# Kernel tuning notes

Hardware: AMD Instinct MI355X
Metric: run time of the kernel (lower is better)

The kernel has to match this reference:

```python
import jax, jax.numpy as jnp
import numpy as np

S, B, H, V = 512, 512, 256, 128


def setup_inputs() -> dict:
    key = jax.random.key(0)
    ks = jax.random.split(key, 11)
    sd = 0.05
    return {
        "x": jax.random.randint(ks[0], (S, B), 0, V, dtype=jnp.int32),
        "w_ih0": jax.random.normal(ks[1], (4 * H, 1), jnp.float32) * sd,
        "w_hh0": jax.random.normal(ks[2], (4 * H, H), jnp.float32) * sd,
        "b_ih0": jax.random.normal(ks[3], (4 * H,), jnp.float32) * sd,
        "b_hh0": jax.random.normal(ks[4], (4 * H,), jnp.float32) * sd,
        "w_ih1": jax.random.normal(ks[5], (4 * H, H), jnp.float32) * sd,
        "w_hh1": jax.random.normal(ks[6], (4 * H, H), jnp.float32) * sd,
        "b_ih1": jax.random.normal(ks[7], (4 * H,), jnp.float32) * sd,
        "b_hh1": jax.random.normal(ks[8], (4 * H,), jnp.float32) * sd,
        "W_out": jax.random.normal(ks[9], (V, H), jnp.float32) * sd,
        "b_out": jax.random.normal(ks[10], (V,), jnp.float32) * sd,
    }


def _lstm_cell(x_t, h, c, w_ih, w_hh, b_ih, b_hh):
    # PyTorch gate order: i, f, g, o
    gates = x_t @ w_ih.T + h @ w_hh.T + b_ih + b_hh  # [B, 4H]
    i, f, g, o = jnp.split(gates, 4, axis=-1)
    c_new = jax.nn.sigmoid(f) * c + jax.nn.sigmoid(i) * jnp.tanh(g)
    h_new = jax.nn.sigmoid(o) * jnp.tanh(c_new)
    return h_new, c_new


def reference(x, w_ih0, w_hh0, b_ih0, b_hh0, w_ih1, w_hh1, b_ih1, b_hh1, W_out, b_out):
    s, b = x.shape
    xf = x.astype(jnp.float32)[..., None]  # [S, B, 1] raw token ids as floats

    def step(carry, x_t):
        h0, c0, h1, c1 = carry
        h0, c0 = _lstm_cell(x_t, h0, c0, w_ih0, w_hh0, b_ih0, b_hh0)
        h1, c1 = _lstm_cell(h0, h1, c1, w_ih1, w_hh1, b_ih1, b_hh1)
        return (h0, c0, h1, c1), h1

    z = jnp.zeros((b, w_hh0.shape[1]), jnp.float32)
    _, hs = jax.lax.scan(step, (z, z, z, z), xf)  # hs: [S, B, H]
    return hs @ W_out.T + b_out  # [S, B, V]
```

## Files before the change

### kernel.cpp

```cpp
#include <hip/hip_runtime.h>


#define S_ 512
#define B_ 512
#define H_ 256
#define V_ 128

typedef _Float16 f16;
typedef __attribute__((ext_vector_type(8))) _Float16 f16x8;
typedef __attribute__((ext_vector_type(4))) float f32x4;
typedef unsigned long long u64;
typedef unsigned u32;
typedef unsigned short u16;

#define OFF_B0   0
#define OFF_B1   524288
#define OFF_BP   1572864
#define OFF_EX   1638400

__device__ __forceinline__ float sigm(float z) { return 1.0f / (1.0f + __expf(-z)); }
__device__ __forceinline__ float tanh_fast(float z) {
  return 2.0f / (1.0f + __expf(-2.0f * z)) - 1.0f;
}

__global__ void prep_kernel(const float* __restrict__ w_hh0,
                            const float* __restrict__ w_ih1, const float* __restrict__ w_hh1,
                            const float* __restrict__ W_out, void* __restrict__ ws) {
  int idx = blockIdx.x * blockDim.x + threadIdx.x;
  f16* wsh = (f16*)ws;
  if (idx < 32768) {
    int j = idx >> 12, w = (idx >> 9) & 7, kk = (idx >> 6) & 7, lane = idx & 63;
    int gate = w >> 1, half = w & 1;
    int hcol = j * 32 + half * 16 + (lane & 15);
    int G = gate * H_ + hcol;
    int k0 = kk * 32 + (lane >> 4) * 8;
    f16x8 v;
    #pragma unroll
    for (int i = 0; i < 8; ++i) v[i] = (f16)w_hh0[G * H_ + k0 + i];
    *(f16x8*)(wsh + idx * 8) = v;
  } else if (idx < 32768 + 65536) {
    int t = idx - 32768;
    int j = t >> 13, w = (t >> 10) & 7, kk = (t >> 6) & 15, lane = t & 63;
    int gate = w >> 1, half = w & 1;
    int hcol = j * 32 + half * 16 + (lane & 15);
    int G = gate * H_ + hcol;
    int k0 = kk * 32 + (lane >> 4) * 8;
    const float* src = (k0 < H_) ? (w_ih1 + G * H_ + k0) : (w_hh1 + G * H_ + (k0 - H_));
    f16x8 v;
    #pragma unroll
    for (int i = 0; i < 8; ++i) v[i] = (f16)src[i];
    *(f16x8*)(wsh + 262144 + t * 8) = v;
  } else if (idx < 32768 + 65536 + 4096) {
    int t = idx - (32768 + 65536);
    int j = t >> 9, w = (t >> 6) & 7, lane = t & 63;
    int vcol = j * 16 + (lane & 15);
    int k0 = w * 32 + (lane >> 4) * 8;
    f16x8 v;
    #pragma unroll
    for (int i = 0; i < 8; ++i) v[i] = (f16)W_out[vcol * H_ + k0 + i];
    *(f16x8*)(wsh + 786432 + t * 8) = v;
  } else if (idx < 102400 + 262144) {
    ((u64*)((char*)ws + OFF_EX))[idx - 102400] = 0ull;
  }
}

__device__ __forceinline__ u64 aload64(const u64* p) {
  return __hip_atomic_load((u64*)p, __ATOMIC_RELAXED, __HIP_MEMORY_SCOPE_AGENT);
}
__device__ __forceinline__ void astore32(u32* p, u32 v) {
  __hip_atomic_store(p, v, __ATOMIC_RELAXED, __HIP_MEMORY_SCOPE_AGENT);
}

__device__ __forceinline__ u32 pack2(u64 q) {
  return (u32)(q & 0xffffu) | (((u32)(q >> 32)) << 16);
}

__device__ __forceinline__ f16x8 afrag(const f16* buf, int lane, int kk) {
  return *(const f16x8*)(buf + kk * 512 + lane * 8);
}

__global__ __launch_bounds__(512, 2) void lstm_r11(const int* __restrict__ x,
                                                   const f16* __restrict__ wts,
                                                   u32* __restrict__ ex,
                                                   const float* __restrict__ w_ih0,
                                                   const float* __restrict__ b_ih0,
                                                   const float* __restrict__ b_hh0,
                                                   const float* __restrict__ b_ih1,
                                                   const float* __restrict__ b_hh1,
                                                   const float* __restrict__ b_out,
                                                   float* __restrict__ out) {
  __shared__ __align__(16) f16 H0[4096], H1[4096];
  __shared__ __align__(16) float gsc0[4][16][33];
  __shared__ __align__(16) float gsc1[4][16][33];
  __shared__ __align__(16) float ppart[4][8][64];

  const int tid  = threadIdx.x;
  const int lane = tid & 63;
  const int w    = tid >> 6;
  const int bg   = blockIdx.x >> 3;
  const int j    = blockIdx.x & 7;

  f16x8 B0r[8], B1r[16], BPr;
  {
    const f16* p0 = wts + (size_t)(j * 8 + w) * 8 * 512 + lane * 8;
    #pragma unroll
    for (int kk = 0; kk < 8; ++kk) B0r[kk] = *(const f16x8*)(p0 + kk * 512);
    const f16* p1 = wts + 262144 + (size_t)(j * 8 + w) * 16 * 512 + lane * 8;
    #pragma unroll
    for (int kk = 0; kk < 16; ++kk) B1r[kk] = *(const f16x8*)(p1 + kk * 512);
    BPr = *(const f16x8*)(wts + 786432 + (size_t)(j * 8 + w) * 512 + lane * 8);
  }

  const int erow = tid >> 5, ecol = tid & 31;
  const int hcol = j * 32 + ecol;
  const int browg = bg * 16 + erow;
  float wxv[4], bz0v[4], bz1v[4];
  #pragma unroll
  for (int g = 0; g < 4; ++g) {
    int G = g * H_ + hcol;
    wxv[g]  = w_ih0[G];
    bz0v[g] = b_ih0[G] + b_hh0[G];
    bz1v[g] = b_ih1[G] + b_hh1[G];
  }
  const float bo = (tid < 256) ? b_out[j * 16 + (tid & 15)] : 0.f;

  u32* exG = ex + (size_t)bg * 16384;

  const int grow = lane & 15;
  const int gcol = w * 32 + ((lane >> 4) << 3);
  const int gidx = grow * 256 + gcol;

  float c0 = 0.f, c1 = 0.f;

  ((u64*)H0)[tid] = 0ull; ((u64*)H0)[tid + 512] = 0ull;
  ((u64*)H1)[tid] = 0ull; ((u64*)H1)[tid + 512] = 0ull;
  __syncthreads();

  #pragma unroll 1
  for (int t = 0; t <= S_ + 1; ++t) {
    float xf = (t < S_) ? (float)x[t * B_ + browg] : 0.f;

    if (t > 0) {
      const u32 want = (u32)t & 0xffffu;
      const u64 pat  = ((u64)want << 16) | ((u64)want << 48);
      const u64 mask = 0xffff0000ffff0000ull;
      const u64* p0 = (const u64*)(exG + ((t - 1) & 1) * 8192 + gidx);
      const u64* p1 = p0 + 2048;
      u64 a0, a1, a2, a3, b0, b1, b2, b3;
      for (;;) {
        a0 = aload64(p0);     a1 = aload64(p0 + 1);
        a2 = aload64(p0 + 2); a3 = aload64(p0 + 3);
        b0 = aload64(p1);     b1 = aload64(p1 + 1);
        b2 = aload64(p1 + 2); b3 = aload64(p1 + 3);
        u64 bad = (a0 ^ pat) | (a1 ^ pat) | (a2 ^ pat) | (a3 ^ pat)
                | (b0 ^ pat) | (b1 ^ pat) | (b2 ^ pat) | (b3 ^ pat);
        if ((bad & mask) == 0) break;
        __builtin_amdgcn_s_sleep(1);
      }
      asm volatile("" ::: "memory");
      u32* d0 = (u32*)H0 + tid * 4;
      u32* d1 = (u32*)H1 + tid * 4;
      d0[0] = pack2(a0); d0[1] = pack2(a1); d0[2] = pack2(a2); d0[3] = pack2(a3);
      d1[0] = pack2(b0); d1[1] = pack2(b1); d1[2] = pack2(b2); d1[3] = pack2(b3);
    }
    __syncthreads();

    {
      f32x4 acc0 = {0.f, 0.f, 0.f, 0.f};
      f32x4 acc1 = {0.f, 0.f, 0.f, 0.f};
      f32x4 ap   = {0.f, 0.f, 0.f, 0.f};
      #pragma unroll
      for (int kk = 0; kk < 8; ++kk) {
        f16x8 ah = afrag(H0, lane, kk);
        acc0 = __builtin_amdgcn_mfma_f32_16x16x32_f16(ah, B0r[kk], acc0, 0, 0, 0);
        acc1 = __builtin_amdgcn_mfma_f32_16x16x32_f16(ah, B1r[kk], acc1, 0, 0, 0);
      }
      #pragma unroll
      for (int kk = 0; kk < 8; ++kk) {
        f16x8 ah = afrag(H1, lane, kk);
        acc1 = __builtin_amdgcn_mfma_f32_16x16x32_f16(ah, B1r[kk + 8], acc1, 0, 0, 0);
      }
      ap = __builtin_amdgcn_mfma_f32_16x16x32_f16(afrag(H1, lane, w), BPr, ap, 0, 0, 0);
      const int gate = w >> 1, half = w & 1;
      const int c16 = lane & 15, r0 = (lane >> 4) * 4;
      #pragma unroll
      for (int r = 0; r < 4; ++r) {
        gsc0[gate][r0 + r][half * 16 + c16] = acc0[r];
        gsc1[gate][r0 + r][half * 16 + c16] = acc1[r];
        ppart[r][w][lane] = ap[r];
      }
    }
    __syncthreads();

    u32* slotW = exG + (t & 1) * 8192;
    const u32 stamp = ((u32)(t + 1) & 0xffffu) << 16;
    if (t <= S_) {
      u32 word = stamp;
      if (t < S_) {
        float gi = gsc0[0][erow][ecol] + xf * wxv[0] + bz0v[0];
        float gf = gsc0[1][erow][ecol] + xf * wxv[1] + bz0v[1];
        float gg = gsc0[2][erow][ecol] + xf * wxv[2] + bz0v[2];
        float go = gsc0[3][erow][ecol] + xf * wxv[3] + bz0v[3];
        c0 = sigm(gf) * c0 + sigm(gi) * tanh_fast(gg);
        float h0 = sigm(go) * tanh_fast(c0);
        union { f16 h; u16 u; } hb; hb.h = (f16)h0;
        word |= (u32)hb.u;
      }
      astore32(slotW + erow * 256 + hcol, word);
    }
    if (t <= S_) {
      float h1 = 0.f;
      if (t >= 1) {
        float gi = gsc1[0][erow][ecol] + bz1v[0];
        float gf = gsc1[1][erow][ecol] + bz1v[1];
        float gg = gsc1[2][erow][ecol] + bz1v[2];
        float go = gsc1[3][erow][ecol] + bz1v[3];
        c1 = sigm(gf) * c1 + sigm(gi) * tanh_fast(gg);
        h1 = sigm(go) * tanh_fast(c1);
      }
      union { f16 h; u16 u; } hb; hb.h = (f16)h1;
      astore32(slotW + 4096 + erow * 256 + hcol, stamp | (u32)hb.u);
    }
    if (t >= 2 && tid < 256) {
      int prow = tid >> 4, pvc = tid & 15;
      int plane = (prow >> 2) * 16 + pvc, preg = prow & 3;
      float s = bo;
      #pragma unroll
      for (int ww = 0; ww < 8; ++ww) s += ppart[preg][ww][plane];
      out[((size_t)((t - 2) * B_ + bg * 16 + prow)) * V_ + j * 16 + pvc] = s;
    }
  }
}

extern "C" void kernel_launch(void* const* d_in, const int* in_sizes, int n_in,
                              void* d_out, int out_size, void* d_ws, size_t ws_size,
                              hipStream_t stream) {
  const int*   x     = (const int*)d_in[0];
  const float* w_ih0 = (const float*)d_in[1];
  const float* w_hh0 = (const float*)d_in[2];
  const float* b_ih0 = (const float*)d_in[3];
  const float* b_hh0 = (const float*)d_in[4];
  const float* w_ih1 = (const float*)d_in[5];
  const float* w_hh1 = (const float*)d_in[6];
  const float* b_ih1 = (const float*)d_in[7];
  const float* b_hh1 = (const float*)d_in[8];
  const float* W_out = (const float*)d_in[9];
  const float* b_out = (const float*)d_in[10];

  prep_kernel<<<1424, 256, 0, stream>>>(w_hh0, w_ih1, w_hh1, W_out, d_ws);

  lstm_r11<<<256, 512, 0, stream>>>(x, (const f16*)d_ws,
                                    (u32*)((char*)d_ws + OFF_EX),
                                    w_ih0, b_ih0, b_hh0, b_ih1, b_hh1, b_out,
                                    (float*)d_out);
}
```

Before: 2.052 ms.

## Pack h0/h1 into one 64-bit stamped word and keep own slice locally

The cross-block exchange now stores h0 and h1 together in a single 64-bit stamped word instead of two 32-bit stores. Each block writes its own hidden-state slice straight into shared memory, and the wave that owns that slice skips polling global memory. The others first spin on a single sentinel word, then load in a wave-wide layout and use a wave vote to exit the retry loop. This is meant to cut global store and poll traffic and the latency of the inter-block handshake, at the cost of more intricate index mapping, which risks subtle layout bugs.

```diff
diff --git a/kernel.cpp b/kernel.cpp
--- a/kernel.cpp
+++ b/kernel.cpp
@@ -67,21 +67,17 @@
 __device__ __forceinline__ u64 aload64(const u64* p) {
   return __hip_atomic_load((u64*)p, __ATOMIC_RELAXED, __HIP_MEMORY_SCOPE_AGENT);
 }
-__device__ __forceinline__ void astore32(u32* p, u32 v) {
+__device__ __forceinline__ void astore64(u64* p, u64 v) {
   __hip_atomic_store(p, v, __ATOMIC_RELAXED, __HIP_MEMORY_SCOPE_AGENT);
-}
-
-__device__ __forceinline__ u32 pack2(u64 q) {
-  return (u32)(q & 0xffffu) | (((u32)(q >> 32)) << 16);
 }
 
 __device__ __forceinline__ f16x8 afrag(const f16* buf, int lane, int kk) {
   return *(const f16x8*)(buf + kk * 512 + lane * 8);
 }
 
-__global__ __launch_bounds__(512, 2) void lstm_r11(const int* __restrict__ x,
+__global__ __launch_bounds__(512, 2) void lstm_r12(const int* __restrict__ x,
                                                    const f16* __restrict__ wts,
-                                                   u32* __restrict__ ex,
+                                                   u64* __restrict__ ex,
                                                    const float* __restrict__ w_ih0,
                                                    const float* __restrict__ b_ih0,
                                                    const float* __restrict__ b_hh0,
@@ -124,11 +120,11 @@
   }
   const float bo = (tid < 256) ? b_out[j * 16 + (tid & 15)] : 0.f;
 
-  u32* exG = ex + (size_t)bg * 16384;
-
-  const int grow = lane & 15;
-  const int gcol = w * 32 + ((lane >> 4) << 3);
-  const int gidx = grow * 256 + gcol;
+  u64* exG = ex + (size_t)bg * 8192;
+
+  const int fij = j * 512 + (erow + 16 * (ecol >> 3)) * 8 + (ecol & 7);
+
+  const int grow2 = lane >> 2;
 
   float c0 = 0.f, c1 = 0.f;
 
@@ -140,28 +136,36 @@
   for (int t = 0; t <= S_ + 1; ++t) {
     float xf = (t < S_) ? (float)x[t * B_ + browg] : 0.f;
 
-    if (t > 0) {
-      const u32 want = (u32)t & 0xffffu;
-      const u64 pat  = ((u64)want << 16) | ((u64)want << 48);
-      const u64 mask = 0xffff0000ffff0000ull;
-      const u64* p0 = (const u64*)(exG + ((t - 1) & 1) * 8192 + gidx);
-      const u64* p1 = p0 + 2048;
-      u64 a0, a1, a2, a3, b0, b1, b2, b3;
+    if (t > 0 && w != j) {
+      const u32 st  = (u32)t & 0xffffu;
+      const u64 pat = ((u64)st << 48) | ((u64)st << 16);
+      const u64 msk = 0xffff0000ffff0000ull;
+      const u64* sb = exG + ((t - 1) & 1) * 4096;
+      while (((aload64(sb + w * 32) ^ pat) & msk) != 0)
+        __builtin_amdgcn_s_sleep(1);
+      asm volatile("" ::: "memory");
+      const u64* base = sb + grow2 * 256 + w * 32 + (lane & 3) * 2;
+      u64 q0, q1, q2, q3, q4, q5, q6, q7;
       for (;;) {
-        a0 = aload64(p0);     a1 = aload64(p0 + 1);
-        a2 = aload64(p0 + 2); a3 = aload64(p0 + 3);
-        b0 = aload64(p1);     b1 = aload64(p1 + 1);
-        b2 = aload64(p1 + 2); b3 = aload64(p1 + 3);
-        u64 bad = (a0 ^ pat) | (a1 ^ pat) | (a2 ^ pat) | (a3 ^ pat)
-                | (b0 ^ pat) | (b1 ^ pat) | (b2 ^ pat) | (b3 ^ pat);
-        if ((bad & mask) == 0) break;
+        q0 = aload64(base);      q1 = aload64(base + 1);
+        q2 = aload64(base + 8);  q3 = aload64(base + 9);
+        q4 = aload64(base + 16); q5 = aload64(base + 17);
+        q6 = aload64(base + 24); q7 = aload64(base + 25);
+        u64 bad = (q0 ^ pat) | (q1 ^ pat) | (q2 ^ pat) | (q3 ^ pat)
+                | (q4 ^ pat) | (q5 ^ pat) | (q6 ^ pat) | (q7 ^ pat);
+        if (!__any((int)((bad & msk) != 0))) break;
         __builtin_amdgcn_s_sleep(1);
       }
-      asm volatile("" ::: "memory");
-      u32* d0 = (u32*)H0 + tid * 4;
-      u32* d1 = (u32*)H1 + tid * 4;
-      d0[0] = pack2(a0); d0[1] = pack2(a1); d0[2] = pack2(a2); d0[3] = pack2(a3);
-      d1[0] = pack2(b0); d1[1] = pack2(b1); d1[2] = pack2(b2); d1[3] = pack2(b3);
+      u32* d0 = (u32*)H0;
+      u32* d1 = (u32*)H1;
+      d0[w * 256 +   0 + lane] = (u32)(q0 & 0xffffu) | ((u32)(q1 & 0xffffu) << 16);
+      d1[w * 256 +   0 + lane] = (u32)((q0 >> 32) & 0xffffu) | ((u32)((q1 >> 32) & 0xffffu) << 16);
+      d0[w * 256 +  64 + lane] = (u32)(q2 & 0xffffu) | ((u32)(q3 & 0xffffu) << 16);
+      d1[w * 256 +  64 + lane] = (u32)((q2 >> 32) & 0xffffu) | ((u32)((q3 >> 32) & 0xffffu) << 16);
+      d0[w * 256 + 128 + lane] = (u32)(q4 & 0xffffu) | ((u32)(q5 & 0xffffu) << 16);
+      d1[w * 256 + 128 + lane] = (u32)((q4 >> 32) & 0xffffu) | ((u32)((q5 >> 32) & 0xffffu) << 16);
+      d0[w * 256 + 192 + lane] = (u32)(q6 & 0xffffu) | ((u32)(q7 & 0xffffu) << 16);
+      d1[w * 256 + 192 + lane] = (u32)((q6 >> 32) & 0xffffu) | ((u32)((q7 >> 32) & 0xffffu) << 16);
     }
     __syncthreads();
 
@@ -192,34 +196,32 @@
     }
     __syncthreads();
 
-    u32* slotW = exG + (t & 1) * 8192;
-    const u32 stamp = ((u32)(t + 1) & 0xffffu) << 16;
     if (t <= S_) {
-      u32 word = stamp;
+      float h0f = 0.f;
       if (t < S_) {
         float gi = gsc0[0][erow][ecol] + xf * wxv[0] + bz0v[0];
         float gf = gsc0[1][erow][ecol] + xf * wxv[1] + bz0v[1];
         float gg = gsc0[2][erow][ecol] + xf * wxv[2] + bz0v[2];
         float go = gsc0[3][erow][ecol] + xf * wxv[3] + bz0v[3];
         c0 = sigm(gf) * c0 + sigm(gi) * tanh_fast(gg);
-        float h0 = sigm(go) * tanh_fast(c0);
-        union { f16 h; u16 u; } hb; hb.h = (f16)h0;
-        word |= (u32)hb.u;
-      }
-      astore32(slotW + erow * 256 + hcol, word);
-    }
-    if (t <= S_) {
-      float h1 = 0.f;
+        h0f = sigm(go) * tanh_fast(c0);
+      }
+      float h1f = 0.f;
       if (t >= 1) {
         float gi = gsc1[0][erow][ecol] + bz1v[0];
         float gf = gsc1[1][erow][ecol] + bz1v[1];
         float gg = gsc1[2][erow][ecol] + bz1v[2];
         float go = gsc1[3][erow][ecol] + bz1v[3];
         c1 = sigm(gf) * c1 + sigm(gi) * tanh_fast(gg);
-        h1 = sigm(go) * tanh_fast(c1);
-      }
-      union { f16 h; u16 u; } hb; hb.h = (f16)h1;
-      astore32(slotW + 4096 + erow * 256 + hcol, stamp | (u32)hb.u);
+        h1f = sigm(go) * tanh_fast(c1);
+      }
+      union { f16 h; u16 u; } ha, hb;
+      ha.h = (f16)h0f; hb.h = (f16)h1f;
+      H0[fij] = ha.h;
+      H1[fij] = hb.h;
+      const u32 st1 = (u32)(t + 1) & 0xffffu;
+      u64 word = ((u64)st1 << 48) | ((u64)hb.u << 32) | ((u64)st1 << 16) | (u64)ha.u;
+      astore64(exG + (t & 1) * 4096 + erow * 256 + hcol, word);
     }
     if (t >= 2 && tid < 256) {
       int prow = tid >> 4, pvc = tid & 15;
@@ -249,8 +251,8 @@
 
   prep_kernel<<<1424, 256, 0, stream>>>(w_hh0, w_ih1, w_hh1, W_out, d_ws);
 
-  lstm_r11<<<256, 512, 0, stream>>>(x, (const f16*)d_ws,
-                                    (u32*)((char*)d_ws + OFF_EX),
+  lstm_r12<<<256, 512, 0, stream>>>(x, (const f16*)d_ws,
+                                    (u64*)((char*)d_ws + OFF_EX),
                                     w_ih0, b_ih0, b_hh0, b_ih1, b_hh1, b_out,
                                     (float*)d_out);
 }
```

Result: faster. 1.806 ms (-12.0%).
